# Kernel tuning notes

Measured on AMD Instinct MI355X. Metric: run time of the kernel, lower is better.

The kernel has to match this reference:

```python
import jax, jax.numpy as jnp
import numpy as np

B, W, C, H = 2, 2048, 1024, 16
K = C // H  # 64
LN_EPS = 1e-5


def setup_inputs() -> dict:
    key = jax.random.key(0)
    ks = jax.random.split(key, 8)
    return {
        "seq1": jax.random.normal(ks[0], (B, W, C), jnp.float32),
        "seq2": jax.random.normal(ks[1], (B, W, C), jnp.float32),
        "ln_gamma": jnp.ones((C,), jnp.float32),
        "ln_beta": jnp.zeros((C,), jnp.float32),
        "q_proj": jax.random.normal(ks[2], (H, C, K), jnp.float32) * 0.02,
        "k_proj": jax.random.normal(ks[3], (H, C, K), jnp.float32) * 0.02,
        "v_proj": jax.random.normal(ks[4], (H, C, K), jnp.float32) * 0.02,
        "mixer_w": jax.random.normal(ks[5], (C, C), jnp.float32) * 0.02,
        "mixer_b": jnp.zeros((C,), jnp.float32),
    }


def _layernorm(x, gamma, beta):
    mu = jnp.mean(x, axis=-1, keepdims=True)
    var = jnp.mean(jnp.square(x - mu), axis=-1, keepdims=True)
    return (x - mu) * jax.lax.rsqrt(var + LN_EPS) * gamma + beta


def reference(seq1, seq2, ln_gamma, ln_beta, q_proj, k_proj, v_proj, mixer_w, mixer_b):
    x1 = _layernorm(seq1, ln_gamma, ln_beta)  # [B,W,C]
    x2 = _layernorm(seq2, ln_gamma, ln_beta)
    # per-head projections: [B,W,C] x [H,C,K] -> [B,H,W,K]
    q = jnp.einsum("bwc,hck->bhwk", x1, q_proj)
    k = jnp.einsum("bwc,hck->bhwk", x2, k_proj)
    v = jnp.einsum("bwc,hck->bhwk", x2, v_proj)
    scores = jnp.einsum("bhqk,bhmk->bhqm", q, k) / jnp.sqrt(jnp.float32(K))
    # causal mask (is_decoder=True)
    causal = jnp.tril(jnp.ones((W, W), bool))
    scores = jnp.where(causal[None, None], scores, jnp.float32(-jnp.inf))
    probs = jax.nn.softmax(scores, axis=-1)
    out = jnp.einsum("bhqm,bhmk->bhqk", probs, v)  # [B,H,W,K]
    out = out.transpose(0, 2, 1, 3).reshape(B, W, C)  # [B,W,C]
    return out @ mixer_w.T + mixer_b
```

## Files before the change

kernel.cpp:

```cpp
#include <hip/hip_runtime.h>
#include <math.h>

#define B_ 2
#define W_ 2048
#define C_ 1024
#define H_ 16
#define K_ 64
#define LN_EPS 1e-5f

typedef __attribute__((ext_vector_type(8))) short short8;
typedef __attribute__((ext_vector_type(4))) float float4v;

#if __has_builtin(__builtin_amdgcn_exp2f)
#define EXP2(x) __builtin_amdgcn_exp2f(x)
#else
#define EXP2(x) exp2f(x)
#endif

__device__ inline unsigned short f2bf(float f) {
  unsigned u = __float_as_uint(f);
  u += 0x7fffu + ((u >> 16) & 1u);
  return (unsigned short)(u >> 16);
}

__device__ inline float max3f(float a, float b, float c) {
  return fmaxf(fmaxf(a, b), c);
}

__device__ __forceinline__ void gload_lds16(const short* g, short* l) {
  __builtin_amdgcn_global_load_lds(
      (const __attribute__((address_space(1))) void*)g,
      (__attribute__((address_space(3))) void*)l, 16, 0, 0);
}

__device__ inline float block_sum(float val) {
  __shared__ float sb[4];
  #pragma unroll
  for (int o = 32; o > 0; o >>= 1) val += __shfl_down(val, o, 64);
  int lane = threadIdx.x & 63, wid = threadIdx.x >> 6;
  if (lane == 0) sb[wid] = val;
  __syncthreads();
  float r = sb[0] + sb[1] + sb[2] + sb[3];
  __syncthreads();
  return r;
}

__global__ __launch_bounds__(256) void ln_kernel(
    const float* __restrict__ seq1, const float* __restrict__ seq2,
    const float* __restrict__ gamma, const float* __restrict__ beta,
    short* __restrict__ x1b, short* __restrict__ x2b) {
  int row = blockIdx.x;
  const int nrows = B_ * W_;
  bool first = row < nrows;
  const float* src = first ? seq1 : seq2;
  short* dst = first ? x1b : x2b;
  int r = first ? row : row - nrows;

  const float4* p = (const float4*)(src + (size_t)r * C_);
  float4 v = p[threadIdx.x];
  float mean = block_sum(v.x + v.y + v.z + v.w) * (1.0f / C_);
  float dx = v.x - mean, dy = v.y - mean, dz = v.z - mean, dw = v.w - mean;
  float var = block_sum(dx * dx + dy * dy + dz * dz + dw * dw) * (1.0f / C_);
  float rstd = rsqrtf(var + LN_EPS);

  float4 g = ((const float4*)gamma)[threadIdx.x];
  float4 b = ((const float4*)beta)[threadIdx.x];
  uint2 o;
  o.x = (unsigned)f2bf(dx * rstd * g.x + b.x) |
        ((unsigned)f2bf(dy * rstd * g.y + b.y) << 16);
  o.y = (unsigned)f2bf(dz * rstd * g.z + b.z) |
        ((unsigned)f2bf(dw * rstd * g.w + b.w) << 16);
  ((uint2*)(dst + (size_t)r * C_))[threadIdx.x] = o;
}

__global__ __launch_bounds__(256) void wprep_proj_kernel(
    const float* __restrict__ qp, const float* __restrict__ kp,
    const float* __restrict__ vp,
    short* __restrict__ wqt, short* __restrict__ wkt, short* __restrict__ wvt) {
  int cb = blockIdx.x, h = blockIdx.y, which = blockIdx.z;
  const float* P = (which == 0 ? qp : (which == 1 ? kp : vp)) + (size_t)h * C_ * K_;
  short* Wt = (which == 0 ? wqt : (which == 1 ? wkt : wvt));
  float scale = (which == 0) ? 0.125f * 1.4426950408889634f : 1.0f;

  __shared__ float Ls[64][65];
  int t = threadIdx.x;
  {
    int cr = t >> 2, ks = (t & 3) * 16;
    const float* src = P + (size_t)(cb * 64 + cr) * K_ + ks;
    #pragma unroll
    for (int j = 0; j < 4; ++j) {
      float4 v = *(const float4*)(src + j * 4);
      Ls[cr][ks + j * 4 + 0] = v.x; Ls[cr][ks + j * 4 + 1] = v.y;
      Ls[cr][ks + j * 4 + 2] = v.z; Ls[cr][ks + j * 4 + 3] = v.w;
    }
  }
  __syncthreads();
  int kr = t >> 2, cs = (t & 3) * 16;
  unsigned u[8];
  #pragma unroll
  for (int i = 0; i < 8; ++i) {
    float a = Ls[cs + 2 * i][kr] * scale;
    float b = Ls[cs + 2 * i + 1][kr] * scale;
    u[i] = (unsigned)f2bf(a) | ((unsigned)f2bf(b) << 16);
  }
  short* dst = Wt + ((size_t)h * 64 + kr) * C_ + cb * 64 + cs;
  uint4 p0; p0.x = u[0]; p0.y = u[1]; p0.z = u[2]; p0.w = u[3];
  uint4 p1; p1.x = u[4]; p1.y = u[5]; p1.z = u[6]; p1.w = u[7];
  *(uint4*)dst = p0;
  *(uint4*)(dst + 8) = p1;
}

__global__ __launch_bounds__(256) void wprep_mix_kernel(
    const float* __restrict__ wm, short* __restrict__ wmb) {
  int gid = blockIdx.x * 256 + threadIdx.x;
  float4 v = ((const float4*)wm)[gid];
  uint2 o;
  o.x = (unsigned)f2bf(v.x) | ((unsigned)f2bf(v.y) << 16);
  o.y = (unsigned)f2bf(v.z) | ((unsigned)f2bf(v.w) << 16);
  ((uint2*)wmb)[gid] = o;
}

__device__ __forceinline__ void gemm_core(
    const short* __restrict__ A, const short* __restrict__ Bt,
    int arow0, int brow0, short* As, short* Bs, float4v acc[4][4]) {
  int tid = threadIdx.x;
  int wave = tid >> 6, lane = tid & 63;
  int lr = lane >> 3, lc = lane & 7;
  int sc = lc ^ lr;
  int wr = wave >> 1, wc = wave & 1;
  int lg = lane >> 4, ll = lane & 15;

  #pragma unroll
  for (int mi = 0; mi < 4; ++mi)
    #pragma unroll
    for (int ni = 0; ni < 4; ++ni) {
      acc[mi][ni][0] = 0.f; acc[mi][ni][1] = 0.f;
      acc[mi][ni][2] = 0.f; acc[mi][ni][3] = 0.f;
    }

  for (int k0 = 0; k0 < C_; k0 += 64) {
    __syncthreads();
    #pragma unroll
    for (int j = 0; j < 4; ++j) {
      int seg = wave * 4 + j;
      int r = seg * 8 + lr;
      gload_lds16(A + (size_t)(arow0 + r) * C_ + k0 + sc * 8, As + seg * 512);
      gload_lds16(Bt + (size_t)(brow0 + r) * C_ + k0 + sc * 8, Bs + seg * 512);
    }
    __syncthreads();
    #pragma unroll
    for (int kc = 0; kc < 2; ++kc) {
      int cc = kc * 4 + lg;
      short8 af[4], bf[4];
      #pragma unroll
      for (int mi = 0; mi < 4; ++mi) {
        int m = wr * 64 + mi * 16 + ll;
        af[mi] = *(const short8*)&As[m * 64 + ((cc ^ (m & 7)) << 3)];
      }
      #pragma unroll
      for (int ni = 0; ni < 4; ++ni) {
        int n = wc * 64 + ni * 16 + ll;
        bf[ni] = *(const short8*)&Bs[n * 64 + ((cc ^ (n & 7)) << 3)];
      }
      #pragma unroll
      for (int mi = 0; mi < 4; ++mi)
        #pragma unroll
        for (int ni = 0; ni < 4; ++ni)
          acc[mi][ni] = __builtin_amdgcn_mfma_f32_16x16x32_bf16(
              af[mi], bf[ni], acc[mi][ni], 0, 0, 0);
    }
  }
}

__device__ __forceinline__ void gemm_core64(
    const short* __restrict__ A, const short* __restrict__ Bt,
    int arow0, int brow0, short* As, short* Bs, float4v acc[2][4]) {
  int tid = threadIdx.x;
  int wave = tid >> 6, lane = tid & 63;
  int lr = lane >> 3, lc = lane & 7;
  int sc = lc ^ lr;
  int wr = wave >> 1, wc = wave & 1;
  int lg = lane >> 4, ll = lane & 15;

  #pragma unroll
  for (int mi = 0; mi < 2; ++mi)
    #pragma unroll
    for (int ni = 0; ni < 4; ++ni) {
      acc[mi][ni][0] = 0.f; acc[mi][ni][1] = 0.f;
      acc[mi][ni][2] = 0.f; acc[mi][ni][3] = 0.f;
    }

  for (int k0 = 0; k0 < C_; k0 += 64) {
    __syncthreads();
    #pragma unroll
    for (int j = 0; j < 2; ++j) {
      int seg = wave * 2 + j;
      int r = seg * 8 + lr;
      gload_lds16(A + (size_t)(arow0 + r) * C_ + k0 + sc * 8, As + seg * 512);
    }
    #pragma unroll
    for (int j = 0; j < 4; ++j) {
      int seg = wave * 4 + j;
      int r = seg * 8 + lr;
      gload_lds16(Bt + (size_t)(brow0 + r) * C_ + k0 + sc * 8, Bs + seg * 512);
    }
    __syncthreads();
    #pragma unroll
    for (int kc = 0; kc < 2; ++kc) {
      int cc = kc * 4 + lg;
      short8 af[2], bf[4];
      #pragma unroll
      for (int mi = 0; mi < 2; ++mi) {
        int m = wr * 32 + mi * 16 + ll;
        af[mi] = *(const short8*)&As[m * 64 + ((cc ^ (m & 7)) << 3)];
      }
      #pragma unroll
      for (int ni = 0; ni < 4; ++ni) {
        int n = wc * 64 + ni * 16 + ll;
        bf[ni] = *(const short8*)&Bs[n * 64 + ((cc ^ (n & 7)) << 3)];
      }
      #pragma unroll
      for (int mi = 0; mi < 2; ++mi)
        #pragma unroll
        for (int ni = 0; ni < 4; ++ni)
          acc[mi][ni] = __builtin_amdgcn_mfma_f32_16x16x32_bf16(
              af[mi], bf[ni], acc[mi][ni], 0, 0, 0);
    }
  }
}

__global__ __launch_bounds__(256, 3) void gemm_qkv_kernel(
    const short* __restrict__ x1b, const short* __restrict__ x2b,
    const short* __restrict__ wqt, const short* __restrict__ wkt,
    const short* __restrict__ wvt,
    short* __restrict__ qb, short* __restrict__ kb, short* __restrict__ vtb) {
  __shared__ short smem[128 * 132];
  short* As = smem;
  short* Bs = smem + 8192;
  int z = blockIdx.z;
  const short *A, *Bt;
  int arow0, brow0;
  if (z == 0)      { A = x1b; Bt = wqt; arow0 = blockIdx.x * 128; brow0 = blockIdx.y * 128; }
  else if (z == 1) { A = x2b; Bt = wkt; arow0 = blockIdx.x * 128; brow0 = blockIdx.y * 128; }
  else             { A = wvt; Bt = x2b; arow0 = blockIdx.y * 128; brow0 = blockIdx.x * 128; }

  float4v acc[4][4];
  gemm_core(A, Bt, arow0, brow0, As, Bs, acc);

  int tid = threadIdx.x;
  int wave = tid >> 6, lane = tid & 63;
  int wr = wave >> 1, wc = wave & 1, lg = lane >> 4, ll = lane & 15;

  __syncthreads();
  #pragma unroll
  for (int mi = 0; mi < 4; ++mi)
    #pragma unroll
    for (int ni = 0; ni < 4; ++ni)
      #pragma unroll
      for (int r2 = 0; r2 < 4; ++r2)
        smem[(wr * 64 + mi * 16 + lg * 4 + r2) * 132 + wc * 64 + ni * 16 + ll] =
            (short)f2bf(acc[mi][ni][r2]);
  __syncthreads();

  if (z <= 1) {
    short* O = (z == 0) ? qb : kb;
    int hb = brow0 >> 6;
    #pragma unroll
    for (int p = 0; p < 8; ++p) {
      int r = p * 16 + (tid >> 4);
      int seg = tid & 15;
      int m = arow0 + r, b = m >> 11, w = m & (W_ - 1);
      int half = seg >> 3, kkseg = seg & 7;
      const short* src = &smem[r * 132 + seg * 8];
      uint2 lo = *(const uint2*)src;
      uint2 hi = *(const uint2*)(src + 4);
      uint4 val; val.x = lo.x; val.y = lo.y; val.z = hi.x; val.w = hi.y;
      *(uint4*)(O + ((size_t)(b * H_ + hb + half) * W_ + w) * K_ + kkseg * 8) = val;
    }
  } else {
    int b = brow0 >> 11, w0 = brow0 & (W_ - 1);
    #pragma unroll
    for (int p = 0; p < 8; ++p) {
      int r = p * 16 + (tid >> 4);
      int seg = tid & 15;
      int mg = arow0 + r, h = mg >> 6, kk = mg & 63;
      const short* src = &smem[r * 132 + seg * 8];
      uint2 lo = *(const uint2*)src;
      uint2 hi = *(const uint2*)(src + 4);
      uint4 val; val.x = lo.x; val.y = lo.y; val.z = hi.x; val.w = hi.y;
      *(uint4*)(vtb + ((size_t)(b * H_ + h) * K_ + kk) * W_ + w0 + seg * 8) = val;
    }
  }
}

__global__ __launch_bounds__(256, 3) void gemm_mix_kernel(
    const short* __restrict__ attnb, const short* __restrict__ wmb,
    const float* __restrict__ bias, float* __restrict__ out) {
  __shared__ short As[64 * 64], Bs[128 * 64];
  int arow0 = blockIdx.x * 64, brow0 = blockIdx.y * 128;
  float4v acc[2][4];
  gemm_core64(attnb, wmb, arow0, brow0, As, Bs, acc);

  int wave = threadIdx.x >> 6, lane = threadIdx.x & 63;
  int wr = wave >> 1, wc = wave & 1, lg = lane >> 4, ll = lane & 15;
  #pragma unroll
  for (int mi = 0; mi < 2; ++mi)
    #pragma unroll
    for (int ni = 0; ni < 4; ++ni) {
      int n = brow0 + wc * 64 + ni * 16 + ll;
      float bv = bias[n];
      #pragma unroll
      for (int r2 = 0; r2 < 4; ++r2) {
        int m = arow0 + wr * 32 + mi * 16 + lg * 4 + r2;
        out[(size_t)m * C_ + n] = acc[mi][ni][r2] + bv;
      }
    }
}

__global__ __launch_bounds__(256, 3) void attn_mfma_kernel(
    const short* __restrict__ q, const short* __restrict__ k,
    const short* __restrict__ vt, short* __restrict__ out) {
  int bh = blockIdx.x;
  int b = bh >> 4, h = bh & 15;
  int s = blockIdx.y;
  int qt = (s < 16) ? (31 - s) : (s - 16);
  int wave = threadIdx.x >> 6;
  int lane = threadIdx.x & 63;
  int lg = lane >> 4, ll = lane & 15;

  __shared__ short Ks[2][64 * 64];
  __shared__ short Vs[2][64 * 64];
  __shared__ short Ps[4][16 * 72];

  const short* qp = q + (size_t)bh * W_ * K_;
  const short* kp = k + (size_t)bh * W_ * K_;
  const short* vb = vt + (size_t)bh * K_ * W_;

  int qrow = qt * 64 + wave * 16 + ll;
  short8 aq[2];
  #pragma unroll
  for (int kc = 0; kc < 2; ++kc)
    aq[kc] = *(const short8*)(qp + (size_t)qrow * K_ + kc * 32 + lg * 8);

  short8 ones;
  #pragma unroll
  for (int i = 0; i < 8; ++i) ones[i] = (short)0x3F80;

  float4v o[4];
  #pragma unroll
  for (int ct = 0; ct < 4; ++ct) {
    o[ct][0] = 0.f; o[ct][1] = 0.f; o[ct][2] = 0.f; o[ct][3] = 0.f;
  }
  float4v lsum;
  lsum[0] = 0.f; lsum[1] = 0.f; lsum[2] = 0.f; lsum[3] = 0.f;
  float m = -INFINITY;

  int nkt = qt + 1;

  #define STAGE(kt, buf)                                                   \
    {                                                                      \
      const short* kbase = kp + (size_t)(kt) * 64 * K_;                    \
      const short* vbase = vb + (kt) * 64;                                 \
      _Pragma("unroll")                                                    \
      for (int j = 0; j < 2; ++j) {                                        \
        int sdx = j * 256 + (int)threadIdx.x;                              \
        int mm = sdx >> 3, c7 = sdx & 7;                                   \
        int gc = c7 ^ (mm & 7);                                            \
        gload_lds16(kbase + (size_t)mm * K_ + gc * 8, &Ks[buf][sdx * 8]);  \
        gload_lds16(vbase + (size_t)mm * W_ + gc * 8, &Vs[buf][sdx * 8]);  \
      }                                                                    \
    }

  STAGE(0, 0);
  for (int kt = 0; kt < nkt; ++kt) {
    int cur = kt & 1;
    if (kt + 1 < nkt) {
      STAGE(kt + 1, cur ^ 1);
      asm volatile("s_waitcnt vmcnt(4)\ns_barrier" ::: "memory");
    } else {
      asm volatile("s_waitcnt vmcnt(0)\ns_barrier" ::: "memory");
    }

    float4v st[4];
    __builtin_amdgcn_s_setprio(1);
    #pragma unroll
    for (int nt = 0; nt < 4; ++nt) {
      st[nt][0] = 0.f; st[nt][1] = 0.f; st[nt][2] = 0.f; st[nt][3] = 0.f;
      int n = nt * 16 + ll;
      #pragma unroll
      for (int kc = 0; kc < 2; ++kc) {
        int cc = kc * 4 + lg;
        short8 bk = *(const short8*)&Ks[cur][n * 64 + ((cc ^ (n & 7)) << 3)];
        st[nt] = __builtin_amdgcn_mfma_f32_16x16x32_bf16(bk, aq[kc], st[nt], 0, 0, 0);
      }
    }
    __builtin_amdgcn_s_setprio(0);

    short8 bv[4][2];
    #pragma unroll
    for (int ct = 0; ct < 4; ++ct) {
      int c = ct * 16 + ll;
      #pragma unroll
      for (int kc = 0; kc < 2; ++kc) {
        int cc = kc * 4 + lg;
        bv[ct][kc] = *(const short8*)&Vs[cur][c * 64 + ((cc ^ (c & 7)) << 3)];
      }
    }

    if (kt == qt) {
      #pragma unroll
      for (int nt = 0; nt < 4; ++nt) {
        int keyb = nt * 16 + lg * 4;
        #pragma unroll
        for (int r = 0; r < 4; ++r)
          if (keyb + r > wave * 16 + ll) st[nt][r] = -INFINITY;
      }
    }

    float ma = max3f(st[0][0], st[0][1], st[0][2]);
    float mb = max3f(st[0][3], st[1][0], st[1][1]);
    float mc = max3f(st[1][2], st[1][3], st[2][0]);
    float md = max3f(st[2][1], st[2][2], st[2][3]);
    float me = max3f(st[3][0], st[3][1], st[3][2]);
    float lm = fmaxf(max3f(ma, mb, mc), max3f(md, me, st[3][3]));
    lm = fmaxf(lm, __shfl_xor(lm, 16, 64));
    lm = fmaxf(lm, __shfl_xor(lm, 32, 64));
    if (!__all(lm <= m + 8.f)) {
      float nm = fmaxf(m, lm);
      float al = EXP2(m - nm);
      m = nm;
      lsum[0] *= al; lsum[1] *= al; lsum[2] *= al; lsum[3] *= al;
      #pragma unroll
      for (int ct = 0; ct < 4; ++ct) {
        o[ct][0] *= al; o[ct][1] *= al; o[ct][2] *= al; o[ct][3] *= al;
      }
    }

    float p[4][4];
    #pragma unroll
    for (int nt = 0; nt < 4; ++nt)
      #pragma unroll
      for (int r = 0; r < 4; ++r)
        p[nt][r] = EXP2(st[nt][r] - m);

    short* myP = &Ps[wave][ll * 72];
    #pragma unroll
    for (int nt = 0; nt < 4; ++nt) {
      uint2 w;
      w.x = (unsigned)f2bf(p[nt][0]) | ((unsigned)f2bf(p[nt][1]) << 16);
      w.y = (unsigned)f2bf(p[nt][2]) | ((unsigned)f2bf(p[nt][3]) << 16);
      *(uint2*)(myP + nt * 16 + lg * 4) = w;
    }
    __builtin_amdgcn_s_waitcnt(0xC07F);
    short8 bp0 = *(const short8*)(myP + lg * 8);
    short8 bp1 = *(const short8*)(myP + 32 + lg * 8);

    __builtin_amdgcn_s_setprio(1);
    lsum = __builtin_amdgcn_mfma_f32_16x16x32_bf16(ones, bp0, lsum, 0, 0, 0);
    lsum = __builtin_amdgcn_mfma_f32_16x16x32_bf16(ones, bp1, lsum, 0, 0, 0);
    #pragma unroll
    for (int ct = 0; ct < 4; ++ct) {
      o[ct] = __builtin_amdgcn_mfma_f32_16x16x32_bf16(bv[ct][0], bp0, o[ct], 0, 0, 0);
      o[ct] = __builtin_amdgcn_mfma_f32_16x16x32_bf16(bv[ct][1], bp1, o[ct], 0, 0, 0);
    }
    __builtin_amdgcn_s_setprio(0);
    asm volatile("s_waitcnt lgkmcnt(0)\ns_barrier" ::: "memory");
  }
  #undef STAGE

  float invl = 1.0f / lsum[0];
  size_t orow = ((size_t)(b * W_ + qrow)) * C_ + h * K_;
  #pragma unroll
  for (int ct = 0; ct < 4; ++ct) {
    uint2 w;
    w.x = (unsigned)f2bf(o[ct][0] * invl) | ((unsigned)f2bf(o[ct][1] * invl) << 16);
    w.y = (unsigned)f2bf(o[ct][2] * invl) | ((unsigned)f2bf(o[ct][3] * invl) << 16);
    *(uint2*)(out + orow + ct * 16 + lg * 4) = w;
  }
}

extern "C" void kernel_launch(void* const* d_in, const int* in_sizes, int n_in,
                              void* d_out, int out_size, void* d_ws, size_t ws_size,
                              hipStream_t stream) {
  const float* seq1  = (const float*)d_in[0];
  const float* seq2  = (const float*)d_in[1];
  const float* gamma = (const float*)d_in[2];
  const float* beta  = (const float*)d_in[3];
  const float* qp    = (const float*)d_in[4];
  const float* kp    = (const float*)d_in[5];
  const float* vp    = (const float*)d_in[6];
  const float* wm    = (const float*)d_in[7];
  const float* mb    = (const float*)d_in[8];
  float* out = (float*)d_out;

  char* ws = (char*)d_ws;
  const size_t NROW = (size_t)B_ * W_;
  const size_t XB = NROW * C_ * sizeof(short);
  const size_t WB = (size_t)C_ * C_ * sizeof(short);
  short* x1b = (short*)(ws);
  short* x2b = (short*)(ws + XB);
  short* qb  = (short*)(ws + 2 * XB);
  short* kb  = (short*)(ws + 3 * XB);
  short* vtb = (short*)(ws + 4 * XB);
  short* wqt = (short*)(ws + 5 * XB);
  short* wkt = (short*)(ws + 5 * XB + WB);
  short* wvt = (short*)(ws + 5 * XB + 2 * WB);
  short* wmb = (short*)(ws + 5 * XB + 3 * WB);
  short* attnb = (short*)(ws + 5 * XB + 4 * WB);

  wprep_proj_kernel<<<dim3(C_ / 64, H_, 3), dim3(256), 0, stream>>>(
      qp, kp, vp, wqt, wkt, wvt);
  wprep_mix_kernel<<<dim3(C_ * C_ / 1024), dim3(256), 0, stream>>>(wm, wmb);
  ln_kernel<<<dim3(2 * (unsigned)NROW), dim3(256), 0, stream>>>(
      seq1, seq2, gamma, beta, x1b, x2b);
  gemm_qkv_kernel<<<dim3(32, 8, 3), dim3(256), 0, stream>>>(
      x1b, x2b, wqt, wkt, wvt, qb, kb, vtb);
  attn_mfma_kernel<<<dim3(32, 32), dim3(256), 0, stream>>>(
      qb, kb, vtb, attnb);
  gemm_mix_kernel<<<dim3(64, 8), dim3(256), 0, stream>>>(attnb, wmb, mb, out);
}
```

Before: 197.4 us.

## Fuse weight-prep kernels, single-pass layernorm stats, one barrier per attention tile

Merges the projection and mixer weight conversion into one launch, removing a kernel launch. Layernorm now computes sum and sum-of-squares in a single block reduction instead of two, halving the barriers and shuffles. The attention loop now waits for all loads and issues one barrier at the top before prefetching the next tile, instead of two barriers per iteration. The single-pass variance can lose precision to cancellation. Issuing the next tile's loads only after the barrier may shrink the overlap between memory traffic and MFMA work.

```diff
diff --git a/kernel.cpp b/kernel.cpp
--- a/kernel.cpp
+++ b/kernel.cpp
@@ -33,14 +33,19 @@
       (__attribute__((address_space(3))) void*)l, 16, 0, 0);
 }
 
-__device__ inline float block_sum(float val) {
-  __shared__ float sb[4];
-  #pragma unroll
-  for (int o = 32; o > 0; o >>= 1) val += __shfl_down(val, o, 64);
+__device__ inline float2 block_sum2(float a, float b) {
+  __shared__ float2 sb[4];
+  #pragma unroll
+  for (int o = 32; o > 0; o >>= 1) {
+    a += __shfl_down(a, o, 64);
+    b += __shfl_down(b, o, 64);
+  }
   int lane = threadIdx.x & 63, wid = threadIdx.x >> 6;
-  if (lane == 0) sb[wid] = val;
+  if (lane == 0) { sb[wid].x = a; sb[wid].y = b; }
   __syncthreads();
-  float r = sb[0] + sb[1] + sb[2] + sb[3];
+  float2 r;
+  r.x = (sb[0].x + sb[1].x) + (sb[2].x + sb[3].x);
+  r.y = (sb[0].y + sb[1].y) + (sb[2].y + sb[3].y);
   __syncthreads();
   return r;
 }
@@ -58,32 +63,50 @@
 
   const float4* p = (const float4*)(src + (size_t)r * C_);
   float4 v = p[threadIdx.x];
-  float mean = block_sum(v.x + v.y + v.z + v.w) * (1.0f / C_);
-  float dx = v.x - mean, dy = v.y - mean, dz = v.z - mean, dw = v.w - mean;
-  float var = block_sum(dx * dx + dy * dy + dz * dz + dw * dw) * (1.0f / C_);
+  float s1 = (v.x + v.y) + (v.z + v.w);
+  float s2 = (v.x * v.x + v.y * v.y) + (v.z * v.z + v.w * v.w);
+  float2 s = block_sum2(s1, s2);
+  float mean = s.x * (1.0f / C_);
+  float var = s.y * (1.0f / C_) - mean * mean;
   float rstd = rsqrtf(var + LN_EPS);
 
   float4 g = ((const float4*)gamma)[threadIdx.x];
   float4 b = ((const float4*)beta)[threadIdx.x];
   uint2 o;
-  o.x = (unsigned)f2bf(dx * rstd * g.x + b.x) |
-        ((unsigned)f2bf(dy * rstd * g.y + b.y) << 16);
-  o.y = (unsigned)f2bf(dz * rstd * g.z + b.z) |
-        ((unsigned)f2bf(dw * rstd * g.w + b.w) << 16);
+  o.x = (unsigned)f2bf((v.x - mean) * rstd * g.x + b.x) |
+        ((unsigned)f2bf((v.y - mean) * rstd * g.y + b.y) << 16);
+  o.y = (unsigned)f2bf((v.z - mean) * rstd * g.z + b.z) |
+        ((unsigned)f2bf((v.w - mean) * rstd * g.w + b.w) << 16);
   ((uint2*)(dst + (size_t)r * C_))[threadIdx.x] = o;
 }
 
-__global__ __launch_bounds__(256) void wprep_proj_kernel(
+__global__ __launch_bounds__(256) void wprep_kernel(
     const float* __restrict__ qp, const float* __restrict__ kp,
-    const float* __restrict__ vp,
-    short* __restrict__ wqt, short* __restrict__ wkt, short* __restrict__ wvt) {
+    const float* __restrict__ vp, const float* __restrict__ wm,
+    short* __restrict__ wqt, short* __restrict__ wkt, short* __restrict__ wvt,
+    short* __restrict__ wmb) {
   int cb = blockIdx.x, h = blockIdx.y, which = blockIdx.z;
+  int t = threadIdx.x;
+
+  if (which == 3) {
+    int blk = h * 16 + cb;
+    #pragma unroll
+    for (int j = 0; j < 4; ++j) {
+      int gid = blk * 1024 + j * 256 + t;
+      float4 v = ((const float4*)wm)[gid];
+      uint2 o;
+      o.x = (unsigned)f2bf(v.x) | ((unsigned)f2bf(v.y) << 16);
+      o.y = (unsigned)f2bf(v.z) | ((unsigned)f2bf(v.w) << 16);
+      ((uint2*)wmb)[gid] = o;
+    }
+    return;
+  }
+
   const float* P = (which == 0 ? qp : (which == 1 ? kp : vp)) + (size_t)h * C_ * K_;
   short* Wt = (which == 0 ? wqt : (which == 1 ? wkt : wvt));
   float scale = (which == 0) ? 0.125f * 1.4426950408889634f : 1.0f;
 
   __shared__ float Ls[64][65];
-  int t = threadIdx.x;
   {
     int cr = t >> 2, ks = (t & 3) * 16;
     const float* src = P + (size_t)(cb * 64 + cr) * K_ + ks;
@@ -108,16 +131,6 @@
   uint4 p1; p1.x = u[4]; p1.y = u[5]; p1.z = u[6]; p1.w = u[7];
   *(uint4*)dst = p0;
   *(uint4*)(dst + 8) = p1;
-}
-
-__global__ __launch_bounds__(256) void wprep_mix_kernel(
-    const float* __restrict__ wm, short* __restrict__ wmb) {
-  int gid = blockIdx.x * 256 + threadIdx.x;
-  float4 v = ((const float4*)wm)[gid];
-  uint2 o;
-  o.x = (unsigned)f2bf(v.x) | ((unsigned)f2bf(v.y) << 16);
-  o.y = (unsigned)f2bf(v.z) | ((unsigned)f2bf(v.w) << 16);
-  ((uint2*)wmb)[gid] = o;
 }
 
 __device__ __forceinline__ void gemm_core(
@@ -374,12 +387,8 @@
   STAGE(0, 0);
   for (int kt = 0; kt < nkt; ++kt) {
     int cur = kt & 1;
-    if (kt + 1 < nkt) {
-      STAGE(kt + 1, cur ^ 1);
-      asm volatile("s_waitcnt vmcnt(4)\ns_barrier" ::: "memory");
-    } else {
-      asm volatile("s_waitcnt vmcnt(0)\ns_barrier" ::: "memory");
-    }
+    asm volatile("s_waitcnt vmcnt(0) lgkmcnt(0)\ns_barrier" ::: "memory");
+    if (kt + 1 < nkt) STAGE(kt + 1, cur ^ 1);
 
     float4v st[4];
     __builtin_amdgcn_s_setprio(1);
@@ -464,7 +473,6 @@
       o[ct] = __builtin_amdgcn_mfma_f32_16x16x32_bf16(bv[ct][1], bp1, o[ct], 0, 0, 0);
     }
     __builtin_amdgcn_s_setprio(0);
-    asm volatile("s_waitcnt lgkmcnt(0)\ns_barrier" ::: "memory");
   }
   #undef STAGE
 
@@ -508,9 +516,8 @@
   short* wmb = (short*)(ws + 5 * XB + 3 * WB);
   short* attnb = (short*)(ws + 5 * XB + 4 * WB);
 
-  wprep_proj_kernel<<<dim3(C_ / 64, H_, 3), dim3(256), 0, stream>>>(
-      qp, kp, vp, wqt, wkt, wvt);
-  wprep_mix_kernel<<<dim3(C_ * C_ / 1024), dim3(256), 0, stream>>>(wm, wmb);
+  wprep_kernel<<<dim3(C_ / 64, H_, 4), dim3(256), 0, stream>>>(
+      qp, kp, vp, wm, wqt, wkt, wvt, wmb);
   ln_kernel<<<dim3(2 * (unsigned)NROW), dim3(256), 0, stream>>>(
       seq1, seq2, gamma, beta, x1b, x2b);
   gemm_qkv_kernel<<<dim3(32, 8, 3), dim3(256), 0, stream>>>(
```

Measured after the change: 193.0 us (median of 2 runs). 2.2% less time.
